# Optimization experiments

Measured on AMD Instinct MI355X. Metric: run time of the kernel, lower is better.

Reference implementation:

```python
import jax, jax.numpy as jnp
import numpy as np

N_NODES = 50000
N_EDGES = 800000
IN_CH = 64
HID_CH = 64
OUT_CH = 64
NUM_GRAPHS = 256


def setup_inputs() -> dict:
    key = jax.random.key(0)
    ks = jax.random.split(key, 9)
    x = jax.random.normal(ks[0], (N_NODES, IN_CH), dtype=jnp.float32)
    edge_index = jax.random.randint(ks[1], (2, N_EDGES), 0, N_NODES, dtype=jnp.int64)
    batch = jnp.sort(jax.random.randint(ks[2], (N_NODES,), 0, NUM_GRAPHS, dtype=jnp.int64))
    def glorot(k, fan_in, fan_out):
        s = jnp.sqrt(6.0 / (fan_in + fan_out))
        return jax.random.uniform(k, (fan_in, fan_out), jnp.float32, -s, s)
    W1 = glorot(ks[3], IN_CH, HID_CH)
    b1 = jnp.zeros((HID_CH,), jnp.float32)
    W2 = glorot(ks[4], HID_CH, HID_CH)
    b2 = jnp.zeros((HID_CH,), jnp.float32)
    W3 = glorot(ks[5], HID_CH, OUT_CH)
    b3 = jnp.zeros((OUT_CH,), jnp.float32)
    return {"x": x, "edge_index": edge_index, "batch": batch,
            "W1": W1, "b1": b1, "W2": W2, "b2": b2, "W3": W3, "b3": b3}


def gcn_conv(x, src, dst, W, b):
    # PyG GCNConv: linear, add self-loops, symmetric deg normalization, scatter-add, bias
    n = x.shape[0]
    xw = x @ W                                   # [N, F_out]
    loops = jnp.arange(n, dtype=src.dtype)
    s = jnp.concatenate([src, loops])            # sources (with self loops)
    d = jnp.concatenate([dst, loops])            # targets (with self loops)
    ones = jnp.ones(d.shape, dtype=x.dtype)
    deg = jax.ops.segment_sum(ones, d, num_segments=n)
    dinv = jnp.where(deg > 0, jax.lax.rsqrt(deg), 0.0)
    norm = dinv[s] * dinv[d]                     # [E + N]
    msgs = norm[:, None] * xw[s]                 # gather + scale
    out = jax.ops.segment_sum(msgs, d, num_segments=n)
    return out + b


def reference(x, edge_index, batch, W1, b1, W2, b2, W3, b3):
    src, dst = edge_index[0], edge_index[1]
    h = jax.nn.relu(gcn_conv(x, src, dst, W1, b1))
    h = jax.nn.relu(gcn_conv(h, src, dst, W2, b2))
    h = gcn_conv(h, src, dst, W3, b3)
    # global_add_pool over graph ids
    pooled = jax.ops.segment_sum(h, batch, num_segments=NUM_GRAPHS)  # [G, OUT_CH]
    return pooled  # out_channels != 1, so no flatten
```

## Files before the change

### kernel.cpp

```cpp
#include <hip/hip_runtime.h>
#include <hip/hip_bf16.h>
#include <hip/hip_fp16.h>

#define N_NODES 50000
#define N_EDGES 800000
#define CH 64
#define N_GRAPHS 256
#define NBUCK 196
#define CHUNK 2048
#define NHIST 98

__device__ __forceinline__ unsigned bf16_rne(float f) {
    unsigned u = __float_as_uint(f);
    return (u + 0x7fffu + ((u >> 16) & 1u)) >> 16;
}
__device__ __forceinline__ float4 ldtab(const unsigned short* __restrict__ tab, int s, int c4) {
    uint2 u = *(const uint2*)(tab + ((size_t)s << 6) + c4);
    float4 r;
    r.x = __uint_as_float(u.x << 16);
    r.y = __uint_as_float(u.x & 0xffff0000u);
    r.z = __uint_as_float(u.y << 16);
    r.w = __uint_as_float(u.y & 0xffff0000u);
    return r;
}
__device__ __forceinline__ unsigned pack_sn(int s, float n) {
    return (unsigned)s | ((unsigned)__half_as_ushort(__float2half_rn(n)) << 16);
}
__device__ __forceinline__ float unpack_n(unsigned p) {
    return __half2float(__ushort_as_half((unsigned short)(p >> 16)));
}

__global__ void edge_hist(const int* __restrict__ ei, int* __restrict__ hpart) {
    __shared__ int h[NBUCK];
    for (int i = threadIdx.x; i < NBUCK; i += 256) h[i] = 0;
    __syncthreads();
    int t = blockIdx.x * 256 + threadIdx.x;
    int stride = NHIST * 256 * 4;
    for (int e = t * 4; e < N_EDGES; e += stride) {
        int4 d = *(const int4*)&ei[N_EDGES + e];
        atomicAdd(&h[d.x >> 8], 1);
        atomicAdd(&h[d.y >> 8], 1);
        atomicAdd(&h[d.z >> 8], 1);
        atomicAdd(&h[d.w >> 8], 1);
    }
    __syncthreads();
    for (int i = threadIdx.x; i < NBUCK; i += 256)
        hpart[blockIdx.x * NBUCK + i] = h[i];
}

__global__ void bucket_scan(const int* __restrict__ hpart, int* __restrict__ bstart,
                            int* __restrict__ gcur, float* __restrict__ poolz) {
    int i = blockIdx.x * 256 + threadIdx.x;
    if (i < N_GRAPHS * CH + N_GRAPHS) poolz[i] = 0.0f;
    if (blockIdx.x != 0) return;
    __shared__ int sc[256];
    int tid = threadIdx.x;
    int v = 0;
    if (tid < NBUCK)
        for (int r = 0; r < NHIST; ++r) v += hpart[r * NBUCK + tid];
    sc[tid] = v;
    __syncthreads();
    for (int off = 1; off < 256; off <<= 1) {
        int t = (tid >= off) ? sc[tid - off] : 0;
        __syncthreads();
        sc[tid] += t;
        __syncthreads();
    }
    if (tid < NBUCK) {
        int ex = sc[tid] - v;
        bstart[tid] = ex;
        gcur[tid] = ex;
    }
    if (tid == 255) bstart[NBUCK] = sc[255];
}

__global__ __launch_bounds__(256) void bin_scatter(const int* __restrict__ ei,
                                                   int* __restrict__ gcur,
                                                   unsigned* __restrict__ ebuf) {
    __shared__ int hist[NBUCK];
    __shared__ int lofs[NBUCK];
    __shared__ int gbase[NBUCK];
    __shared__ int cur[NBUCK];
    __shared__ int sc[256];
    __shared__ unsigned stage[CHUNK];
    int tid = threadIdx.x;
    for (int i = tid; i < NBUCK; i += 256) hist[i] = 0;
    __syncthreads();
    int e0 = blockIdx.x * CHUNK;
    int n = min(CHUNK, N_EDGES - e0);
    int src[8], dst[8];
#pragma unroll
    for (int k = 0; k < 8; ++k) {
        int idx = k * 256 + tid;
        if (idx < n) {
            int e = e0 + idx;
            src[k] = ei[e];
            dst[k] = ei[N_EDGES + e];
            atomicAdd(&hist[dst[k] >> 8], 1);
        } else dst[k] = -1;
    }
    __syncthreads();
    int v = (tid < NBUCK) ? hist[tid] : 0;
    sc[tid] = v;
    __syncthreads();
    for (int off = 1; off < 256; off <<= 1) {
        int t = (tid >= off) ? sc[tid - off] : 0;
        __syncthreads();
        sc[tid] += t;
        __syncthreads();
    }
    if (tid < NBUCK) {
        int ex = sc[tid] - v;
        lofs[tid] = ex;
        cur[tid] = ex;
        gbase[tid] = v ? atomicAdd(&gcur[tid], v) : 0;
    }
    __syncthreads();
#pragma unroll
    for (int k = 0; k < 8; ++k) {
        if (dst[k] >= 0) {
            int b = dst[k] >> 8;
            int p = atomicAdd(&cur[b], 1);
            stage[p] = (unsigned)src[k] | ((unsigned)(dst[k] & 255) << 16)
                                        | ((unsigned)b << 24);
        }
    }
    __syncthreads();
    for (int i = tid; i < n; i += 256) {
        unsigned p = stage[i];
        int b = p >> 24;
        ebuf[gbase[b] + (i - lofs[b])] = p;
    }
}

__global__ void csr_bucket(const unsigned* __restrict__ ebuf, const int* __restrict__ bstart,
                           int* __restrict__ deg, int* __restrict__ rowp,
                           float* __restrict__ dinv, int* __restrict__ col) {
    __shared__ int nd[256];
    __shared__ int cur[256];
    __shared__ int sc[256];
    int b = blockIdx.x;
    int tid = threadIdx.x;
    nd[tid] = 0;
    __syncthreads();
    int es = bstart[b], ee = bstart[b + 1];
    for (int e = es + tid; e < ee; e += 256)
        atomicAdd(&nd[(ebuf[e] >> 16) & 255], 1);
    __syncthreads();
    int v = nd[tid];
    sc[tid] = v;
    __syncthreads();
    for (int off = 1; off < 256; off <<= 1) {
        int t = (tid >= off) ? sc[tid - off] : 0;
        __syncthreads();
        sc[tid] += t;
        __syncthreads();
    }
    int node = b * 256 + tid;
    int lstart = es + sc[tid] - v;
    if (node < N_NODES) {
        deg[node] = v;
        rowp[node] = lstart;
        dinv[node] = rsqrtf((float)v + 1.0f);
    }
    cur[tid] = lstart;
    __syncthreads();
    for (int e = es + tid; e < ee; e += 256) {
        unsigned p = ebuf[e];
        int pos = atomicAdd(&cur[(p >> 16) & 255], 1);
        col[pos] = (int)(p & 0xFFFFu);
    }
}

template <int IN_BF16>
__global__ void gemm_reg(const void* __restrict__ inv, const float* __restrict__ W,
                         unsigned short* __restrict__ out, int n) {
    __shared__ float WT[64 * 68];
    int tid = threadIdx.x;
    for (int i = tid; i < 64 * 64; i += 256) {
        int k = i >> 6, c = i & 63;
        WT[c * 68 + k] = W[i];
    }
    __syncthreads();
    int lane = tid & 63;
    int wv = __builtin_amdgcn_readfirstlane(tid >> 6);
    int row0 = blockIdx.x * 32 + wv * 8;
    if (row0 >= n) return;
    float acc[8] = {0.f, 0.f, 0.f, 0.f, 0.f, 0.f, 0.f, 0.f};
    if (IN_BF16) {
        const unsigned short* in = (const unsigned short*)inv;
#pragma unroll 2
        for (int k = 0; k < 64; k += 8) {
            float4 w0 = *(const float4*)&WT[lane * 68 + k];
            float4 w1 = *(const float4*)&WT[lane * 68 + k + 4];
#pragma unroll
            for (int r = 0; r < 8; ++r) {
                uint4 xb = *(const uint4*)&in[(size_t)(row0 + r) * 64 + k];
                acc[r] = fmaf(__uint_as_float(xb.x << 16),         w0.x, acc[r]);
                acc[r] = fmaf(__uint_as_float(xb.x & 0xffff0000u), w0.y, acc[r]);
                acc[r] = fmaf(__uint_as_float(xb.y << 16),         w0.z, acc[r]);
                acc[r] = fmaf(__uint_as_float(xb.y & 0xffff0000u), w0.w, acc[r]);
                acc[r] = fmaf(__uint_as_float(xb.z << 16),         w1.x, acc[r]);
                acc[r] = fmaf(__uint_as_float(xb.z & 0xffff0000u), w1.y, acc[r]);
                acc[r] = fmaf(__uint_as_float(xb.w << 16),         w1.z, acc[r]);
                acc[r] = fmaf(__uint_as_float(xb.w & 0xffff0000u), w1.w, acc[r]);
            }
        }
    } else {
        const float* in = (const float*)inv;
#pragma unroll 2
        for (int k = 0; k < 64; k += 4) {
            float4 w = *(const float4*)&WT[lane * 68 + k];
#pragma unroll
            for (int r = 0; r < 8; ++r) {
                float4 xv = *(const float4*)&in[(size_t)(row0 + r) * 64 + k];
                acc[r] = fmaf(xv.x, w.x, acc[r]);
                acc[r] = fmaf(xv.y, w.y, acc[r]);
                acc[r] = fmaf(xv.z, w.z, acc[r]);
                acc[r] = fmaf(xv.w, w.w, acc[r]);
            }
        }
    }
#pragma unroll
    for (int r = 0; r < 8; ++r)
        out[(size_t)(row0 + r) * 64 + lane] = (unsigned short)bf16_rne(acc[r]);
}

template <int OUT_BF16, int USE_PCK, int WRITE_PCK>
__global__ void agg_v4(const int* __restrict__ rowp, const int* __restrict__ deg,
                       const int* __restrict__ col, const float* __restrict__ dinv,
                       unsigned* __restrict__ pck,
                       const unsigned short* __restrict__ tab, const float* __restrict__ bias,
                       void* __restrict__ outv, int do_relu) {
    int wv = __builtin_amdgcn_readfirstlane(threadIdx.x >> 6);
    int node = blockIdx.x * 4 + wv;
    int lane = threadIdx.x & 63;
    int q = lane >> 4;
    int c4 = (lane & 15) << 2;
    float dd = dinv[node];
    int cnt = deg[node];
    int start = rowp[node];
    float4 acc = make_float4(0.f, 0.f, 0.f, 0.f);
    if (q == 0) {
        float4 xs = ldtab(tab, node, c4);
        float dd2 = dd * dd;
        acc.x = xs.x * dd2; acc.y = xs.y * dd2; acc.z = xs.z * dd2; acc.w = xs.w * dd2;
    }
    int j = 0;
    for (; j + 16 <= cnt; j += 16) {
        int s[4]; float nv[4];
#pragma unroll
        for (int u = 0; u < 4; ++u) {
            int idx = start + j + 4 * u + q;
            if (USE_PCK) {
                unsigned p = pck[idx];
                s[u] = (int)(p & 0xFFFFu);
                nv[u] = unpack_n(p);
            } else {
                s[u] = col[idx];
                nv[u] = dinv[s[u]] * dd;
                if (WRITE_PCK && (lane & 15) == 0) pck[idx] = pack_sn(s[u], nv[u]);
            }
        }
#pragma unroll
        for (int u = 0; u < 4; ++u) {
            float4 xv = ldtab(tab, s[u], c4);
            acc.x = fmaf(nv[u], xv.x, acc.x); acc.y = fmaf(nv[u], xv.y, acc.y);
            acc.z = fmaf(nv[u], xv.z, acc.z); acc.w = fmaf(nv[u], xv.w, acc.w);
        }
    }
    for (; j + 8 <= cnt; j += 8) {
        int s[2]; float nv[2];
#pragma unroll
        for (int u = 0; u < 2; ++u) {
            int idx = start + j + 4 * u + q;
            if (USE_PCK) {
                unsigned p = pck[idx];
                s[u] = (int)(p & 0xFFFFu);
                nv[u] = unpack_n(p);
            } else {
                s[u] = col[idx];
                nv[u] = dinv[s[u]] * dd;
                if (WRITE_PCK && (lane & 15) == 0) pck[idx] = pack_sn(s[u], nv[u]);
            }
        }
#pragma unroll
        for (int u = 0; u < 2; ++u) {
            float4 xv = ldtab(tab, s[u], c4);
            acc.x = fmaf(nv[u], xv.x, acc.x); acc.y = fmaf(nv[u], xv.y, acc.y);
            acc.z = fmaf(nv[u], xv.z, acc.z); acc.w = fmaf(nv[u], xv.w, acc.w);
        }
    }
    for (; j < cnt; j += 4) {
        int jj = j + q;
        bool valid = jj < cnt;
        int s; float nv;
        if (USE_PCK) {
            unsigned p = pck[start + (valid ? jj : 0)];
            s = (int)(p & 0xFFFFu);
            nv = valid ? unpack_n(p) : 0.0f;
        } else {
            s = col[start + (valid ? jj : 0)];
            nv = valid ? dinv[s] * dd : 0.0f;
            if (WRITE_PCK && valid && (lane & 15) == 0) pck[start + jj] = pack_sn(s, nv);
        }
        float4 xv = ldtab(tab, s, c4);
        acc.x = fmaf(nv, xv.x, acc.x); acc.y = fmaf(nv, xv.y, acc.y);
        acc.z = fmaf(nv, xv.z, acc.z); acc.w = fmaf(nv, xv.w, acc.w);
    }
    acc.x += __shfl_xor(acc.x, 16); acc.y += __shfl_xor(acc.y, 16);
    acc.z += __shfl_xor(acc.z, 16); acc.w += __shfl_xor(acc.w, 16);
    acc.x += __shfl_xor(acc.x, 32); acc.y += __shfl_xor(acc.y, 32);
    acc.z += __shfl_xor(acc.z, 32); acc.w += __shfl_xor(acc.w, 32);
    if (q == 0) {
        if (bias) {
            float4 bv = *(const float4*)&bias[c4];
            acc.x += bv.x; acc.y += bv.y; acc.z += bv.z; acc.w += bv.w;
        }
        if (do_relu) {
            acc.x = fmaxf(acc.x, 0.f); acc.y = fmaxf(acc.y, 0.f);
            acc.z = fmaxf(acc.z, 0.f); acc.w = fmaxf(acc.w, 0.f);
        }
        if (OUT_BF16) {
            uint2 o;
            o.x = bf16_rne(acc.x) | (bf16_rne(acc.y) << 16);
            o.y = bf16_rne(acc.z) | (bf16_rne(acc.w) << 16);
            *(uint2*)&((unsigned short*)outv)[((size_t)node << 6) + c4] = o;
        } else {
            *(float4*)&((float*)outv)[((size_t)node << 6) + c4] = acc;
        }
    }
}

__global__ void pool_seg(const unsigned short* __restrict__ h, const int* __restrict__ batch,
                         float* __restrict__ pool, float* __restrict__ cntg) {
    int ch = threadIdx.x & 63;
    int grp = threadIdx.x >> 6;
    int base = (blockIdx.x * 4 + grp) * 16;
    float acc = 0.0f;
    int curg = -1, runlen = 0;
    for (int n = 0; n < 16; ++n) {
        int node = base + n;
        if (node >= N_NODES) break;
        int g = batch[node];
        float v = __uint_as_float(((unsigned)h[((size_t)node << 6) + ch]) << 16);
        if (g != curg) {
            if (curg >= 0) {
                atomicAdd(&pool[curg * 64 + ch], acc);
                if (ch == 0) atomicAdd(&cntg[curg], (float)runlen);
            }
            curg = g; acc = v; runlen = 1;
        } else { acc += v; runlen++; }
    }
    if (curg >= 0) {
        atomicAdd(&pool[curg * 64 + ch], acc);
        if (ch == 0) atomicAdd(&cntg[curg], (float)runlen);
    }
}

__global__ void out_gemm(const float* __restrict__ P, const float* __restrict__ cntg,
                         const float* __restrict__ W, const float* __restrict__ b,
                         float* __restrict__ out) {
    __shared__ float Ws[64 * 64];
    int tid = threadIdx.x;
    for (int i = tid; i < 64 * 64; i += 256) Ws[i] = W[i];
    __syncthreads();
    int lane = tid & 63;
    int g = blockIdx.x * 4 + (tid >> 6);
    if (g >= N_GRAPHS) return;
    float pv = P[g * 64 + lane];
    float acc = 0.0f;
#pragma unroll
    for (int k = 0; k < 64; ++k)
        acc = fmaf(__shfl(pv, k, 64), Ws[k * 64 + lane], acc);
    out[g * 64 + lane] = acc + cntg[g] * b[lane];
}

extern "C" void kernel_launch(void* const* d_in, const int* in_sizes, int n_in,
                              void* d_out, int out_size, void* d_ws, size_t ws_size,
                              hipStream_t stream) {
    const float* x   = (const float*)d_in[0];
    const int* ei    = (const int*)d_in[1];
    const int* batch = (const int*)d_in[2];
    const float* W1  = (const float*)d_in[3];
    const float* b1  = (const float*)d_in[4];
    const float* W2  = (const float*)d_in[5];
    const float* b2  = (const float*)d_in[6];
    const float* W3  = (const float*)d_in[7];
    const float* b3  = (const float*)d_in[8];
    float* out = (float*)d_out;

    char* ws = (char*)d_ws;
    float*    dinv  = (float*)(ws);
    int*      DEG   = (int*)(ws + 200192);
    int*      ROWP  = (int*)(ws + 400384);
    int*      COL   = (int*)(ws + 600576);
    unsigned* PCK   = (unsigned*)(ws + 3800576);
    int*      HPART = (int*)(ws + 7000576);
    int*      BST   = (int*)(ws + 7077888);
    int*      GCUR  = (int*)(ws + 7078912);
    float*    XW    = (float*)(ws + 7080960);
    unsigned* EBUF  = (unsigned*)(ws + 7080960);
    float*    ACC   = (float*)(ws + 19880960);
    float*    POOL  = (float*)(ws + 32680960);
    float*    CNT   = (float*)(ws + 32746496);

    const int WAVE_NODE_BLK = N_NODES / 4;
    const int GEMM_BLK = (N_NODES + 31) / 32;
    const int SCAT_BLK = (N_EDGES + CHUNK - 1) / CHUNK;

    edge_hist<<<NHIST, 256, 0, stream>>>(ei, HPART);
    bucket_scan<<<65, 256, 0, stream>>>(HPART, BST, GCUR, POOL);
    bin_scatter<<<SCAT_BLK, 256, 0, stream>>>(ei, GCUR, EBUF);
    csr_bucket<<<NBUCK, 256, 0, stream>>>(EBUF, BST, DEG, ROWP, dinv, COL);

    gemm_reg<0><<<GEMM_BLK, 256, 0, stream>>>(x, W1, (unsigned short*)XW, N_NODES);
    agg_v4<1, 0, 1><<<WAVE_NODE_BLK, 256, 0, stream>>>(ROWP, DEG, COL, dinv, PCK,
        (const unsigned short*)XW, b1, ACC, 1);

    gemm_reg<1><<<GEMM_BLK, 256, 0, stream>>>(ACC, W2, (unsigned short*)XW, N_NODES);
    agg_v4<1, 1, 0><<<WAVE_NODE_BLK, 256, 0, stream>>>(ROWP, DEG, COL, dinv, PCK,
        (const unsigned short*)XW, b2, ACC, 1);

    agg_v4<1, 1, 0><<<WAVE_NODE_BLK, 256, 0, stream>>>(ROWP, DEG, COL, dinv, PCK,
        (const unsigned short*)ACC, nullptr, XW, 0);
    pool_seg<<<(N_NODES + 63) / 64, 256, 0, stream>>>((const unsigned short*)XW,
        batch, POOL, CNT);
    out_gemm<<<N_GRAPHS / 4, 256, 0, stream>>>(POOL, CNT, W3, b3, out);
}
```

Before: 244.3 us.

## Drop edge histogram pass via fixed-capacity buckets and fuse layer-1 GEMM with scatter

Removes the edge_hist and bucket_scan kernels by giving each destination bucket a fixed padded capacity (MAXB slots) in the edge buffer, so scatter blocks can claim space directly with atomics on per-bucket cursors initialised to b*MAXB. The binning scatter and the first-layer x@W1 GEMM are merged into one launch, with blocks split by index and shared memory held in a union, so the two independent jobs overlap. The CSR build reads bucket ends from the final cursors. This saves two launches and a full pass over the destination indices. In exchange it assumes no bucket ever holds more than MAXB edges, which holds only for roughly uniform random degrees, and it needs a larger workspace.

New measurement: 231.4 us. -5.3%, faster.

```diff
diff --git a/kernel.cpp b/kernel.cpp
--- a/kernel.cpp
+++ b/kernel.cpp
@@ -7,8 +7,11 @@
 #define CH 64
 #define N_GRAPHS 256
 #define NBUCK 196
+#define MAXB 4608
+#define NPAD (NBUCK * MAXB)
 #define CHUNK 2048
-#define NHIST 98
+#define SCAT_BLK ((N_EDGES + CHUNK - 1) / CHUNK)
+#define GEMM_BLK ((N_NODES + 31) / 32)
 
 __device__ __forceinline__ unsigned bf16_rne(float f) {
     unsigned u = __float_as_uint(f);
@@ -30,110 +33,103 @@
     return __half2float(__ushort_as_half((unsigned short)(p >> 16)));
 }
 
-__global__ void edge_hist(const int* __restrict__ ei, int* __restrict__ hpart) {
-    __shared__ int h[NBUCK];
-    for (int i = threadIdx.x; i < NBUCK; i += 256) h[i] = 0;
-    __syncthreads();
-    int t = blockIdx.x * 256 + threadIdx.x;
-    int stride = NHIST * 256 * 4;
-    for (int e = t * 4; e < N_EDGES; e += stride) {
-        int4 d = *(const int4*)&ei[N_EDGES + e];
-        atomicAdd(&h[d.x >> 8], 1);
-        atomicAdd(&h[d.y >> 8], 1);
-        atomicAdd(&h[d.z >> 8], 1);
-        atomicAdd(&h[d.w >> 8], 1);
-    }
-    __syncthreads();
-    for (int i = threadIdx.x; i < NBUCK; i += 256)
-        hpart[blockIdx.x * NBUCK + i] = h[i];
-}
-
-__global__ void bucket_scan(const int* __restrict__ hpart, int* __restrict__ bstart,
-                            int* __restrict__ gcur, float* __restrict__ poolz) {
+__global__ void init_k(int* __restrict__ gcur, float* __restrict__ poolz) {
     int i = blockIdx.x * 256 + threadIdx.x;
     if (i < N_GRAPHS * CH + N_GRAPHS) poolz[i] = 0.0f;
-    if (blockIdx.x != 0) return;
-    __shared__ int sc[256];
+    if (i < NBUCK) gcur[i] = i * MAXB;
+}
+
+union FusedSh {
+    struct { float WT[64 * 68]; } g;
+    struct {
+        int hist[NBUCK]; int lofs[NBUCK]; int gbase[NBUCK]; int cur[NBUCK];
+        int sc[256]; unsigned stage[CHUNK];
+    } s;
+};
+__global__ __launch_bounds__(256) void gemm1_scatter(
+        const float* __restrict__ x, const float* __restrict__ W1,
+        unsigned short* __restrict__ xwout,
+        const int* __restrict__ ei, int* __restrict__ gcur, unsigned* __restrict__ ebuf) {
+    __shared__ FusedSh sh;
     int tid = threadIdx.x;
-    int v = 0;
-    if (tid < NBUCK)
-        for (int r = 0; r < NHIST; ++r) v += hpart[r * NBUCK + tid];
-    sc[tid] = v;
-    __syncthreads();
-    for (int off = 1; off < 256; off <<= 1) {
-        int t = (tid >= off) ? sc[tid - off] : 0;
-        __syncthreads();
-        sc[tid] += t;
-        __syncthreads();
-    }
-    if (tid < NBUCK) {
-        int ex = sc[tid] - v;
-        bstart[tid] = ex;
-        gcur[tid] = ex;
-    }
-    if (tid == 255) bstart[NBUCK] = sc[255];
-}
-
-__global__ __launch_bounds__(256) void bin_scatter(const int* __restrict__ ei,
-                                                   int* __restrict__ gcur,
-                                                   unsigned* __restrict__ ebuf) {
-    __shared__ int hist[NBUCK];
-    __shared__ int lofs[NBUCK];
-    __shared__ int gbase[NBUCK];
-    __shared__ int cur[NBUCK];
-    __shared__ int sc[256];
-    __shared__ unsigned stage[CHUNK];
-    int tid = threadIdx.x;
-    for (int i = tid; i < NBUCK; i += 256) hist[i] = 0;
-    __syncthreads();
-    int e0 = blockIdx.x * CHUNK;
-    int n = min(CHUNK, N_EDGES - e0);
-    int src[8], dst[8];
-#pragma unroll
-    for (int k = 0; k < 8; ++k) {
-        int idx = k * 256 + tid;
-        if (idx < n) {
-            int e = e0 + idx;
-            src[k] = ei[e];
-            dst[k] = ei[N_EDGES + e];
-            atomicAdd(&hist[dst[k] >> 8], 1);
-        } else dst[k] = -1;
-    }
-    __syncthreads();
-    int v = (tid < NBUCK) ? hist[tid] : 0;
-    sc[tid] = v;
-    __syncthreads();
-    for (int off = 1; off < 256; off <<= 1) {
-        int t = (tid >= off) ? sc[tid - off] : 0;
-        __syncthreads();
-        sc[tid] += t;
-        __syncthreads();
-    }
-    if (tid < NBUCK) {
-        int ex = sc[tid] - v;
-        lofs[tid] = ex;
-        cur[tid] = ex;
-        gbase[tid] = v ? atomicAdd(&gcur[tid], v) : 0;
-    }
-    __syncthreads();
-#pragma unroll
-    for (int k = 0; k < 8; ++k) {
-        if (dst[k] >= 0) {
-            int b = dst[k] >> 8;
-            int p = atomicAdd(&cur[b], 1);
-            stage[p] = (unsigned)src[k] | ((unsigned)(dst[k] & 255) << 16)
-                                        | ((unsigned)b << 24);
-        }
-    }
-    __syncthreads();
-    for (int i = tid; i < n; i += 256) {
-        unsigned p = stage[i];
-        int b = p >> 24;
-        ebuf[gbase[b] + (i - lofs[b])] = p;
-    }
-}
-
-__global__ void csr_bucket(const unsigned* __restrict__ ebuf, const int* __restrict__ bstart,
+    if (blockIdx.x < SCAT_BLK) {
+        for (int i = tid; i < NBUCK; i += 256) sh.s.hist[i] = 0;
+        __syncthreads();
+        int e0 = blockIdx.x * CHUNK;
+        int n = min(CHUNK, N_EDGES - e0);
+        int src[8], dst[8];
+#pragma unroll
+        for (int k = 0; k < 8; ++k) {
+            int idx = k * 256 + tid;
+            if (idx < n) {
+                int e = e0 + idx;
+                src[k] = ei[e];
+                dst[k] = ei[N_EDGES + e];
+                atomicAdd(&sh.s.hist[dst[k] >> 8], 1);
+            } else dst[k] = -1;
+        }
+        __syncthreads();
+        int v = (tid < NBUCK) ? sh.s.hist[tid] : 0;
+        sh.s.sc[tid] = v;
+        __syncthreads();
+        for (int off = 1; off < 256; off <<= 1) {
+            int t = (tid >= off) ? sh.s.sc[tid - off] : 0;
+            __syncthreads();
+            sh.s.sc[tid] += t;
+            __syncthreads();
+        }
+        if (tid < NBUCK) {
+            int ex = sh.s.sc[tid] - v;
+            sh.s.lofs[tid] = ex;
+            sh.s.cur[tid] = ex;
+            sh.s.gbase[tid] = v ? atomicAdd(&gcur[tid], v) : 0;
+        }
+        __syncthreads();
+#pragma unroll
+        for (int k = 0; k < 8; ++k) {
+            if (dst[k] >= 0) {
+                int b = dst[k] >> 8;
+                int p = atomicAdd(&sh.s.cur[b], 1);
+                sh.s.stage[p] = (unsigned)src[k] | ((unsigned)(dst[k] & 255) << 16)
+                                                | ((unsigned)b << 24);
+            }
+        }
+        __syncthreads();
+        for (int i = tid; i < n; i += 256) {
+            unsigned p = sh.s.stage[i];
+            int b = p >> 24;
+            ebuf[sh.s.gbase[b] + (i - sh.s.lofs[b])] = p;
+        }
+    } else {
+        for (int i = tid; i < 64 * 64; i += 256) {
+            int k = i >> 6, c = i & 63;
+            sh.g.WT[c * 68 + k] = W1[i];
+        }
+        __syncthreads();
+        int lane = tid & 63;
+        int wv = __builtin_amdgcn_readfirstlane(tid >> 6);
+        int row0 = (blockIdx.x - SCAT_BLK) * 32 + wv * 8;
+        if (row0 >= N_NODES) return;
+        float acc[8] = {0.f, 0.f, 0.f, 0.f, 0.f, 0.f, 0.f, 0.f};
+#pragma unroll 2
+        for (int k = 0; k < 64; k += 4) {
+            float4 w = *(const float4*)&sh.g.WT[lane * 68 + k];
+#pragma unroll
+            for (int r = 0; r < 8; ++r) {
+                float4 xv = *(const float4*)&x[(size_t)(row0 + r) * 64 + k];
+                acc[r] = fmaf(xv.x, w.x, acc[r]);
+                acc[r] = fmaf(xv.y, w.y, acc[r]);
+                acc[r] = fmaf(xv.z, w.z, acc[r]);
+                acc[r] = fmaf(xv.w, w.w, acc[r]);
+            }
+        }
+#pragma unroll
+        for (int r = 0; r < 8; ++r)
+            xwout[(size_t)(row0 + r) * 64 + lane] = (unsigned short)bf16_rne(acc[r]);
+    }
+}
+
+__global__ void csr_bucket(const unsigned* __restrict__ ebuf, const int* __restrict__ gcur,
                            int* __restrict__ deg, int* __restrict__ rowp,
                            float* __restrict__ dinv, int* __restrict__ col) {
     __shared__ int nd[256];
@@ -143,7 +139,7 @@
     int tid = threadIdx.x;
     nd[tid] = 0;
     __syncthreads();
-    int es = bstart[b], ee = bstart[b + 1];
+    int es = b * MAXB, ee = gcur[b];
     for (int e = es + tid; e < ee; e += 256)
         atomicAdd(&nd[(ebuf[e] >> 16) & 255], 1);
     __syncthreads();
@@ -172,9 +168,9 @@
     }
 }
 
-template <int IN_BF16>
-__global__ void gemm_reg(const void* __restrict__ inv, const float* __restrict__ W,
-                         unsigned short* __restrict__ out, int n) {
+__global__ void gemm_reg_bf16(const unsigned short* __restrict__ in,
+                              const float* __restrict__ W,
+                              unsigned short* __restrict__ out, int n) {
     __shared__ float WT[64 * 68];
     int tid = threadIdx.x;
     for (int i = tid; i < 64 * 64; i += 256) {
@@ -187,38 +183,21 @@
     int row0 = blockIdx.x * 32 + wv * 8;
     if (row0 >= n) return;
     float acc[8] = {0.f, 0.f, 0.f, 0.f, 0.f, 0.f, 0.f, 0.f};
-    if (IN_BF16) {
-        const unsigned short* in = (const unsigned short*)inv;
 #pragma unroll 2
-        for (int k = 0; k < 64; k += 8) {
-            float4 w0 = *(const float4*)&WT[lane * 68 + k];
-            float4 w1 = *(const float4*)&WT[lane * 68 + k + 4];
-#pragma unroll
-            for (int r = 0; r < 8; ++r) {
-                uint4 xb = *(const uint4*)&in[(size_t)(row0 + r) * 64 + k];
-                acc[r] = fmaf(__uint_as_float(xb.x << 16),         w0.x, acc[r]);
-                acc[r] = fmaf(__uint_as_float(xb.x & 0xffff0000u), w0.y, acc[r]);
-                acc[r] = fmaf(__uint_as_float(xb.y << 16),         w0.z, acc[r]);
-                acc[r] = fmaf(__uint_as_float(xb.y & 0xffff0000u), w0.w, acc[r]);
-                acc[r] = fmaf(__uint_as_float(xb.z << 16),         w1.x, acc[r]);
-                acc[r] = fmaf(__uint_as_float(xb.z & 0xffff0000u), w1.y, acc[r]);
-                acc[r] = fmaf(__uint_as_float(xb.w << 16),         w1.z, acc[r]);
-                acc[r] = fmaf(__uint_as_float(xb.w & 0xffff0000u), w1.w, acc[r]);
-            }
-        }
-    } else {
-        const float* in = (const float*)inv;
-#pragma unroll 2
-        for (int k = 0; k < 64; k += 4) {
-            float4 w = *(const float4*)&WT[lane * 68 + k];
-#pragma unroll
-            for (int r = 0; r < 8; ++r) {
-                float4 xv = *(const float4*)&in[(size_t)(row0 + r) * 64 + k];
-                acc[r] = fmaf(xv.x, w.x, acc[r]);
-                acc[r] = fmaf(xv.y, w.y, acc[r]);
-                acc[r] = fmaf(xv.z, w.z, acc[r]);
-                acc[r] = fmaf(xv.w, w.w, acc[r]);
-            }
+    for (int k = 0; k < 64; k += 8) {
+        float4 w0 = *(const float4*)&WT[lane * 68 + k];
+        float4 w1 = *(const float4*)&WT[lane * 68 + k + 4];
+#pragma unroll
+        for (int r = 0; r < 8; ++r) {
+            uint4 xb = *(const uint4*)&in[(size_t)(row0 + r) * 64 + k];
+            acc[r] = fmaf(__uint_as_float(xb.x << 16),         w0.x, acc[r]);
+            acc[r] = fmaf(__uint_as_float(xb.x & 0xffff0000u), w0.y, acc[r]);
+            acc[r] = fmaf(__uint_as_float(xb.y << 16),         w0.z, acc[r]);
+            acc[r] = fmaf(__uint_as_float(xb.y & 0xffff0000u), w0.w, acc[r]);
+            acc[r] = fmaf(__uint_as_float(xb.z << 16),         w1.x, acc[r]);
+            acc[r] = fmaf(__uint_as_float(xb.z & 0xffff0000u), w1.y, acc[r]);
+            acc[r] = fmaf(__uint_as_float(xb.w << 16),         w1.z, acc[r]);
+            acc[r] = fmaf(__uint_as_float(xb.w & 0xffff0000u), w1.w, acc[r]);
         }
     }
 #pragma unroll
@@ -226,12 +205,12 @@
         out[(size_t)(row0 + r) * 64 + lane] = (unsigned short)bf16_rne(acc[r]);
 }
 
-template <int OUT_BF16, int USE_PCK, int WRITE_PCK>
+template <int USE_PCK, int WRITE_PCK>
 __global__ void agg_v4(const int* __restrict__ rowp, const int* __restrict__ deg,
                        const int* __restrict__ col, const float* __restrict__ dinv,
                        unsigned* __restrict__ pck,
                        const unsigned short* __restrict__ tab, const float* __restrict__ bias,
-                       void* __restrict__ outv, int do_relu) {
+                       unsigned short* __restrict__ outv, int do_relu) {
     int wv = __builtin_amdgcn_readfirstlane(threadIdx.x >> 6);
     int node = blockIdx.x * 4 + wv;
     int lane = threadIdx.x & 63;
@@ -321,14 +300,10 @@
             acc.x = fmaxf(acc.x, 0.f); acc.y = fmaxf(acc.y, 0.f);
             acc.z = fmaxf(acc.z, 0.f); acc.w = fmaxf(acc.w, 0.f);
         }
-        if (OUT_BF16) {
-            uint2 o;
-            o.x = bf16_rne(acc.x) | (bf16_rne(acc.y) << 16);
-            o.y = bf16_rne(acc.z) | (bf16_rne(acc.w) << 16);
-            *(uint2*)&((unsigned short*)outv)[((size_t)node << 6) + c4] = o;
-        } else {
-            *(float4*)&((float*)outv)[((size_t)node << 6) + c4] = acc;
-        }
+        uint2 o;
+        o.x = bf16_rne(acc.x) | (bf16_rne(acc.y) << 16);
+        o.y = bf16_rne(acc.z) | (bf16_rne(acc.w) << 16);
+        *(uint2*)&outv[((size_t)node << 6) + c4] = o;
     }
 }
 
@@ -391,39 +366,37 @@
     float* out = (float*)d_out;
 
     char* ws = (char*)d_ws;
-    float*    dinv  = (float*)(ws);
-    int*      DEG   = (int*)(ws + 200192);
-    int*      ROWP  = (int*)(ws + 400384);
-    int*      COL   = (int*)(ws + 600576);
-    unsigned* PCK   = (unsigned*)(ws + 3800576);
-    int*      HPART = (int*)(ws + 7000576);
-    int*      BST   = (int*)(ws + 7077888);
-    int*      GCUR  = (int*)(ws + 7078912);
-    float*    XW    = (float*)(ws + 7080960);
-    unsigned* EBUF  = (unsigned*)(ws + 7080960);
-    float*    ACC   = (float*)(ws + 19880960);
-    float*    POOL  = (float*)(ws + 32680960);
-    float*    CNT   = (float*)(ws + 32746496);
+    float*    dinv = (float*)(ws);
+    int*      DEG  = (int*)(ws + 200192);
+    int*      ROWP = (int*)(ws + 400384);
+    int*      COL  = (int*)(ws + 600576);
+    unsigned* PCK  = (unsigned*)(ws + 4213248);
+    float*    XW   = (float*)(ws + 7825920);
+    float*    ACC  = (float*)(ws + 20625920);
+    float*    POOL = (float*)(ws + 33425920);
+    float*    CNT  = (float*)(ws + 33491456);
+    int*      GCUR = (int*)(ws + 33492480);
+    unsigned* EBUF = (unsigned*)(ws + 33493504);
 
     const int WAVE_NODE_BLK = N_NODES / 4;
-    const int GEMM_BLK = (N_NODES + 31) / 32;
-    const int SCAT_BLK = (N_EDGES + CHUNK - 1) / CHUNK;
-
-    edge_hist<<<NHIST, 256, 0, stream>>>(ei, HPART);
-    bucket_scan<<<65, 256, 0, stream>>>(HPART, BST, GCUR, POOL);
-    bin_scatter<<<SCAT_BLK, 256, 0, stream>>>(ei, GCUR, EBUF);
-    csr_bucket<<<NBUCK, 256, 0, stream>>>(EBUF, BST, DEG, ROWP, dinv, COL);
-
-    gemm_reg<0><<<GEMM_BLK, 256, 0, stream>>>(x, W1, (unsigned short*)XW, N_NODES);
-    agg_v4<1, 0, 1><<<WAVE_NODE_BLK, 256, 0, stream>>>(ROWP, DEG, COL, dinv, PCK,
-        (const unsigned short*)XW, b1, ACC, 1);
-
-    gemm_reg<1><<<GEMM_BLK, 256, 0, stream>>>(ACC, W2, (unsigned short*)XW, N_NODES);
-    agg_v4<1, 1, 0><<<WAVE_NODE_BLK, 256, 0, stream>>>(ROWP, DEG, COL, dinv, PCK,
-        (const unsigned short*)XW, b2, ACC, 1);
-
-    agg_v4<1, 1, 0><<<WAVE_NODE_BLK, 256, 0, stream>>>(ROWP, DEG, COL, dinv, PCK,
-        (const unsigned short*)ACC, nullptr, XW, 0);
+
+    init_k<<<66, 256, 0, stream>>>(GCUR, POOL);
+
+    gemm1_scatter<<<SCAT_BLK + GEMM_BLK, 256, 0, stream>>>(
+        x, W1, (unsigned short*)XW, ei, GCUR, EBUF);
+
+    csr_bucket<<<NBUCK, 256, 0, stream>>>(EBUF, GCUR, DEG, ROWP, dinv, COL);
+
+    agg_v4<0, 1><<<WAVE_NODE_BLK, 256, 0, stream>>>(ROWP, DEG, COL, dinv, PCK,
+        (const unsigned short*)XW, b1, (unsigned short*)ACC, 1);
+
+    gemm_reg_bf16<<<GEMM_BLK, 256, 0, stream>>>((const unsigned short*)ACC, W2,
+        (unsigned short*)XW, N_NODES);
+    agg_v4<1, 0><<<WAVE_NODE_BLK, 256, 0, stream>>>(ROWP, DEG, COL, dinv, PCK,
+        (const unsigned short*)XW, b2, (unsigned short*)ACC, 1);
+
+    agg_v4<1, 0><<<WAVE_NODE_BLK, 256, 0, stream>>>(ROWP, DEG, COL, dinv, PCK,
+        (const unsigned short*)ACC, nullptr, (unsigned short*)XW, 0);
     pool_seg<<<(N_NODES + 63) / 64, 256, 0, stream>>>((const unsigned short*)XW,
         batch, POOL, CNT);
     out_gemm<<<N_GRAPHS / 4, 256, 0, stream>>>(POOL, CNT, W3, b3, out);
```
